# Kernel tuning notes

Measured on AMD Instinct MI355X. Metric: run time of the kernel, lower is better.

Reference implementation:

```python
import jax, jax.numpy as jnp
import numpy as np

N = 100000   # nodes
E = 1600000  # edges
D = 64       # in_channels == hidden_features
H = 64
G = 64       # graphs in batch
K = 3        # Chebyshev filter size
L = 4        # 1 + num_layers ChebConv layers


def setup_inputs() -> dict:
    key = jax.random.key(0)
    ks = jax.random.split(key, 10)
    x = jax.random.normal(ks[0], (N, D), dtype=jnp.float32)
    edge_index = jax.random.randint(ks[1], (2, E), 0, N, dtype=jnp.int64)
    edge_weight = jax.random.uniform(ks[2], (E,), dtype=jnp.float32)
    batch = jnp.sort(jax.random.randint(ks[3], (N,), 0, G, dtype=jnp.int64))
    s = 1.0 / np.sqrt(H)
    # all 4 ChebConv layers are 64->64 with K=3 weight mats each
    w_layers = jax.random.normal(ks[4], (L, K, D, H), dtype=jnp.float32) * s
    b_layers = jax.random.normal(ks[5], (L, H), dtype=jnp.float32) * 0.01
    # MLPReadout: 64 -> 32 -> 1
    wr1 = jax.random.normal(ks[6], (H, H // 2), dtype=jnp.float32) * s
    br1 = jnp.zeros((H // 2,), dtype=jnp.float32)
    wr2 = jax.random.normal(ks[7], (H // 2, 1), dtype=jnp.float32) * (1.0 / np.sqrt(H // 2))
    br2 = jnp.zeros((1,), dtype=jnp.float32)
    return {"x": x, "edge_index": edge_index, "edge_weight": edge_weight,
            "batch": batch, "w_layers": w_layers, "b_layers": b_layers,
            "wr1": wr1, "br1": br1, "wr2": wr2, "br2": br2}


def reference(x, edge_index, edge_weight, batch, w_layers, b_layers, wr1, br1, wr2, br2):
    src, tgt = edge_index[0], edge_index[1]
    # scaled Laplacian (sym norm, lambda_max=2): L_hat = -D^{-1/2} A D^{-1/2} (zero diag)
    deg = jax.ops.segment_sum(edge_weight, src, num_segments=N)
    dis = jnp.where(deg > 0, jax.lax.rsqrt(jnp.where(deg > 0, deg, 1.0)), 0.0)
    wn = -dis[src] * edge_weight * dis[tgt]  # [E]

    def prop(h):  # h: [N, F] -> L_hat @ h via gather/scatter
        return jax.ops.segment_sum(wn[:, None] * h[src], tgt, num_segments=N)

    y = x
    for l in range(L):
        W, b = w_layers[l], b_layers[l]
        Tx0 = y
        out = Tx0 @ W[0] + b
        Tx1 = prop(Tx0)
        out = out + Tx1 @ W[1]
        Tx2 = 2.0 * prop(Tx1) - Tx0
        out = out + Tx2 @ W[2]
        y = out
    # MLP readout
    h = jax.nn.relu(y @ wr1 + br1)
    r = h @ wr2 + br2  # [N, 1]
    # scatter-mean pooling over graphs
    sums = jax.ops.segment_sum(r, batch, num_segments=G)
    cnt = jax.ops.segment_sum(jnp.ones((N, 1), r.dtype), batch, num_segments=G)
    return sums / jnp.maximum(cnt, 1.0)
```

## Files before the change

### kernel.cpp

```cpp
#include <hip/hip_runtime.h>
#include <hip/hip_bf16.h>


typedef __hip_bfloat16 bf16;
typedef short short8 __attribute__((ext_vector_type(8)));
typedef float floatx4 __attribute__((ext_vector_type(4)));

static __device__ float bf2f(bf16 v){ return __bfloat162float(v); }

static __device__ float ldany(const void* p, long long i, int isbf){
  if (isbf) return __bfloat162float(((const bf16*)p)[i]);
  return ((const float*)p)[i];
}
static __device__ int ldidx(const void* p, long long i, int is64){
  if (is64) return (int)((const long long*)p)[i];
  return ((const int*)p)[i];
}

__global__ void Petri_Cheb_GNN_76639396430230_kernel(){}


__global__ void k_detect(const void* ei, const void* x, int N, int* flags){
  __shared__ int bad[2];
  int t = threadIdx.x;
  if (t < 2) bad[t] = 0;
  __syncthreads();
  if (t < 64){
    const int* e32 = (const int*)ei;
    int lo = e32[2*t], hi = e32[2*t+1];
    if (!(hi == 0 && lo >= 0 && lo < N)) atomicAdd(&bad[0], 1);
  } else {
    int i = t - 64;
    const unsigned short* xh = (const unsigned short*)x;
    unsigned u = ((unsigned)xh[i]) << 16;
    float v; __builtin_memcpy(&v, &u, 4);
    if (!(v == v) || fabsf(v) > 64.f) atomicAdd(&bad[1], 1);
  }
  __syncthreads();
  if (t == 0){ flags[0] = bad[0] ? 0 : 1; flags[1] = bad[1] ? 0 : 1; }
}


__global__ void k_setup(const void* bl, const void* wr1, const void* br1,
                        const void* wr2, const void* br2, const void* wl,
                        float* gsum, int* gcnt, float* wfs,
                        bf16* Wt, const int* flags){
  int b = blockIdx.x;
  int tid = threadIdx.x;
  if (b == 0){
    if (tid < 64){ gsum[tid] = 0.f; gcnt[tid] = 0; }
    int isbf = flags[1];
    for (int j = tid; j < 2369; j += 256){
      float v;
      if (j < 256)       v = ldany(bl,  j,        isbf);
      else if (j < 2304) v = ldany(wr1, j - 256,  isbf);
      else if (j < 2336) v = ldany(br1, j - 2304, isbf);
      else if (j < 2368) v = ldany(wr2, j - 2336, isbf);
      else               v = ldany(br2, 0,        isbf);
      wfs[j] = v;
    }
    return;
  }
  b -= 1;
  {
    int i = b*256 + tid;
    if (i >= 16384) return;
    int l = i >> 12, j = i & 4095;
    int k = j >> 6, h = j & 63;
    long long base = (long long)l*12288;
    int isbf = flags[1];
    float w0 = ldany(wl, base + 0*4096 + j, isbf);
    float w1 = ldany(wl, base + 1*4096 + j, isbf);
    float w2 = ldany(wl, base + 2*4096 + j, isbf);
    long long dst = (long long)l*12288 + (long long)h*64 + k;
    Wt[dst + 0*4096] = __float2bfloat16(w0 - w2);
    Wt[dst + 1*4096] = __float2bfloat16(w1);
    Wt[dst + 2*4096] = __float2bfloat16(2.f * w2);
  }
}

__global__ void k_x2a(const void* x, bf16* a, int n, const int* flags){
  int i = blockIdx.x*256 + threadIdx.x;
  if (i < n) a[i] = __float2bfloat16(ldany(x, i, flags[1]));
}


__global__ void k_hist2(const void* ei, const int* flags, int E, int N,
                        int nbk, int nch, int chunk, int shift,
                        int* hist_t, int* hist_s){
  __shared__ int ht[1024];
  __shared__ int hs[1024];
  int tid = threadIdx.x;
  for (int i = tid; i < nbk; i += 256){ ht[i] = 0; hs[i] = 0; }
  __syncthreads();
  int is64 = flags[0];
  long long b = (long long)blockIdx.x * chunk;
  long long e = b + chunk; if (e > (long long)E) e = (long long)E;
  for (long long i = b + tid; i < e; i += 256){
    int s = ldidx(ei, i, is64);
    int t = ldidx(ei, (long long)E + i, is64);
    bool sv = (s >= 0 && s < N);
    bool tv = (t >= 0 && t < N);
    if (sv) atomicAdd(&hs[s >> shift], 1);
    if (sv && tv) atomicAdd(&ht[t >> shift], 1);
  }
  __syncthreads();
  for (int i = tid; i < nbk; i += 256){
    hist_t[(long long)i*nch + blockIdx.x] = ht[i];
    hist_s[(long long)i*nch + blockIdx.x] = hs[i];
  }
}


__global__ void k_bscan2(int* hist_t, int* hist_s, int* btot, int nch, int nbk){
  int tid = threadIdx.x;
  int bk  = blockIdx.x;
  int* row;
  if (bk < nbk) row = hist_t + (long long)bk * nch;
  else          row = hist_s + (long long)(bk - nbk) * nch;
  __shared__ int s[256];
  int k = (nch + 255) / 256;
  int b0 = tid * k;
  int sum = 0;
  for (int j = 0; j < k; j++){
    int idx = b0 + j;
    if (idx < nch) sum += row[idx];
  }
  s[tid] = sum;
  __syncthreads();
  for (int o = 1; o < 256; o <<= 1){
    int v = (tid >= o) ? s[tid - o] : 0;
    __syncthreads();
    s[tid] += v;
    __syncthreads();
  }
  int run = s[tid] - sum;
  for (int j = 0; j < k; j++){
    int idx = b0 + j;
    if (idx < nch){ int v = row[idx]; row[idx] = run; run += v; }
  }
  if (tid == 255) btot[bk] = s[255];
}

__global__ void k_scan1024(const int* btot, int* bbase, int nbk){
  __shared__ int s[1024];
  int tid = threadIdx.x;
  int off = blockIdx.x * nbk;
  int v = (tid < nbk) ? btot[off + tid] : 0;
  s[tid] = v;
  __syncthreads();
  for (int o = 1; o < 1024; o <<= 1){
    int u = (tid >= o) ? s[tid - o] : 0;
    __syncthreads();
    s[tid] += u;
    __syncthreads();
  }
  if (tid < nbk) bbase[off + tid] = s[tid] - v;
}


__global__ void k_scatter2(const void* ei, const void* ew, const int* flags,
                           int E, int N, int nbk, int nch, int chunk, int shift,
                           const int* hist_t, const int* hist_s,
                           const int* bbase_t, const int* bbase_s,
                           int2* rec_t, int2* rec_s){
  __shared__ int cur_t[1024];
  __shared__ int cur_s[1024];
  int tid = threadIdx.x;
  for (int i = tid; i < nbk; i += 256){
    cur_t[i] = bbase_t[i] + hist_t[(long long)i*nch + blockIdx.x];
    cur_s[i] = bbase_s[i] + hist_s[(long long)i*nch + blockIdx.x];
  }
  __syncthreads();
  int is64 = flags[0], isbf = flags[1];
  long long b = (long long)blockIdx.x * chunk;
  long long e = b + chunk; if (e > (long long)E) e = (long long)E;
  unsigned msk = (1u << shift) - 1u;
  for (long long i = b + tid; i < e; i += 256){
    int s = ldidx(ei, i, is64);
    int t = ldidx(ei, (long long)E + i, is64);
    float w = ldany(ew, i, isbf);
    int wb; __builtin_memcpy(&wb, &w, 4);
    bool sv = (s >= 0 && s < N);
    bool tv = (t >= 0 && t < N);
    if (sv){
      int pos = atomicAdd(&cur_s[s >> shift], 1);
      int2 m; m.x = (int)(s & (int)msk); m.y = wb;
      rec_s[pos] = m;
    }
    if (sv && tv){
      int pos = atomicAdd(&cur_t[t >> shift], 1);
      int2 m; m.x = s | (((int)(t & msk)) << 20); m.y = wb;
      rec_t[pos] = m;
    }
  }
}


__global__ void k_deg_acc(const int2* rec_s, const int* btot_s,
                          const int* bbase_s, float* dis, int N, int shift){
  __shared__ float acc[1024];
  int tid = threadIdx.x;
  int bk  = blockIdx.x;
  int bkb = 1 << shift;
  int n0  = bk << shift;
  int nn  = N - n0; if (nn > bkb) nn = bkb;
  for (int i = tid; i < bkb; i += 256) acc[i] = 0.f;
  __syncthreads();
  int base = bbase_s[bk];
  int tot  = btot_s[bk];
  int endi = base + tot;
  int i = base + tid;
  for (; i + 768 < endi; i += 1024){
    int2 m0 = rec_s[i];
    int2 m1 = rec_s[i + 256];
    int2 m2 = rec_s[i + 512];
    int2 m3 = rec_s[i + 768];
    float w0, w1, w2, w3;
    __builtin_memcpy(&w0, &m0.y, 4);
    __builtin_memcpy(&w1, &m1.y, 4);
    __builtin_memcpy(&w2, &m2.y, 4);
    __builtin_memcpy(&w3, &m3.y, 4);
    atomicAdd(&acc[m0.x], w0);
    atomicAdd(&acc[m1.x], w1);
    atomicAdd(&acc[m2.x], w2);
    atomicAdd(&acc[m3.x], w3);
  }
  for (; i < endi; i += 256){
    int2 m = rec_s[i];
    float w; __builtin_memcpy(&w, &m.y, 4);
    atomicAdd(&acc[m.x], w);
  }
  __syncthreads();
  for (int j = tid; j < nn; j += 256){
    float d = acc[j];
    dis[n0 + j] = (d > 0.f) ? rsqrtf(d) : 0.f;
  }
}


__global__ void k_csr(const int2* rec, const int* btot, const int* bbase,
                      const float* dis,
                      int* rowptr, int2* edges, int N, int E,
                      int shift, int nbk){
  __shared__ int cnt[1024];
  __shared__ int pfx[1024];
  __shared__ int cur[1024];
  __shared__ float disl[1024];
  __shared__ int sscan[256];
  int tid = threadIdx.x;
  int bk  = blockIdx.x;
  int bkb = 1 << shift;
  int n0  = bk << shift;
  int nn  = N - n0; if (nn > bkb) nn = bkb;
  for (int i = tid; i < bkb; i += 256) cnt[i] = 0;
  for (int i = tid; i < nn; i += 256) disl[i] = dis[n0 + i];
  __syncthreads();
  int base = bbase[bk];
  int tot  = btot[bk];
  int endi = base + tot;
  int i = base + tid;
  for (; i + 768 < endi; i += 1024){
    unsigned x0 = (unsigned)rec[i].x;
    unsigned x1 = (unsigned)rec[i + 256].x;
    unsigned x2 = (unsigned)rec[i + 512].x;
    unsigned x3 = (unsigned)rec[i + 768].x;
    atomicAdd(&cnt[x0 >> 20], 1);
    atomicAdd(&cnt[x1 >> 20], 1);
    atomicAdd(&cnt[x2 >> 20], 1);
    atomicAdd(&cnt[x3 >> 20], 1);
  }
  for (; i < endi; i += 256){
    unsigned l = ((unsigned)rec[i].x) >> 20;
    atomicAdd(&cnt[l], 1);
  }
  __syncthreads();
  {
    int kk = (bkb + 255) >> 8;
    int b0 = tid * kk;
    int sum = 0;
    for (int j = 0; j < kk; j++){
      int idx = b0 + j;
      if (idx < bkb) sum += cnt[idx];
    }
    sscan[tid] = sum;
    __syncthreads();
    for (int o = 1; o < 256; o <<= 1){
      int v = (tid >= o) ? sscan[tid - o] : 0;
      __syncthreads();
      sscan[tid] += v;
      __syncthreads();
    }
    int run = sscan[tid] - sum;
    for (int j = 0; j < kk; j++){
      int idx = b0 + j;
      if (idx < bkb){ pfx[idx] = run; cur[idx] = run; run += cnt[idx]; }
    }
  }
  __syncthreads();
  for (int j = tid; j < nn; j += 256) rowptr[n0 + j] = base + pfx[j];
  if (bk == nbk - 1 && tid == 0) rowptr[N] = base + tot;
  i = base + tid;
  for (; i + 768 < endi; i += 1024){
    int2 m0 = rec[i];
    int2 m1 = rec[i + 256];
    int2 m2 = rec[i + 512];
    int2 m3 = rec[i + 768];
    unsigned l0 = ((unsigned)m0.x) >> 20; int s0 = m0.x & 0xFFFFF;
    unsigned l1 = ((unsigned)m1.x) >> 20; int s1 = m1.x & 0xFFFFF;
    unsigned l2 = ((unsigned)m2.x) >> 20; int s2 = m2.x & 0xFFFFF;
    unsigned l3 = ((unsigned)m3.x) >> 20; int s3 = m3.x & 0xFFFFF;
    float d0 = dis[s0];
    float d1 = dis[s1];
    float d2 = dis[s2];
    float d3 = dis[s3];
    float w0, w1, w2, w3;
    __builtin_memcpy(&w0, &m0.y, 4);
    __builtin_memcpy(&w1, &m1.y, 4);
    __builtin_memcpy(&w2, &m2.y, 4);
    __builtin_memcpy(&w3, &m3.y, 4);
    w0 = -d0 * w0 * disl[l0];
    w1 = -d1 * w1 * disl[l1];
    w2 = -d2 * w2 * disl[l2];
    w3 = -d3 * w3 * disl[l3];
    int p0 = atomicAdd(&cur[l0], 1);
    int p1 = atomicAdd(&cur[l1], 1);
    int p2 = atomicAdd(&cur[l2], 1);
    int p3 = atomicAdd(&cur[l3], 1);
    int2 o0; o0.x = s0; __builtin_memcpy(&o0.y, &w0, 4);
    int2 o1; o1.x = s1; __builtin_memcpy(&o1.y, &w1, 4);
    int2 o2; o2.x = s2; __builtin_memcpy(&o2.y, &w2, 4);
    int2 o3; o3.x = s3; __builtin_memcpy(&o3.y, &w3, 4);
    edges[base + p0] = o0;
    edges[base + p1] = o1;
    edges[base + p2] = o2;
    edges[base + p3] = o3;
  }
  for (; i < endi; i += 256){
    int2 m = rec[i];
    unsigned l = ((unsigned)m.x) >> 20;
    int s = m.x & 0xFFFFF;
    float w; __builtin_memcpy(&w, &m.y, 4);
    w = -dis[s] * w * disl[l];
    int pos = atomicAdd(&cur[l], 1);
    int2 o; o.x = s; __builtin_memcpy(&o.y, &w, 4);
    edges[base + pos] = o;
  }
}


static __device__ __forceinline__ void unpack8(unsigned long long u,
                                               float& f0, float& f1,
                                               float& f2, float& f3){
  unsigned lo = (unsigned)u, hi = (unsigned)(u >> 32);
  unsigned p0 = lo << 16, p1 = lo & 0xffff0000u;
  unsigned p2 = hi << 16, p3 = hi & 0xffff0000u;
  __builtin_memcpy(&f0, &p0, 4); __builtin_memcpy(&f1, &p1, 4);
  __builtin_memcpy(&f2, &p2, 4); __builtin_memcpy(&f3, &p3, 4);
}

__global__ void k_prop(const int* rowptr, const int2* edges,
                       const bf16* hin, bf16* hout, int N){
  __shared__ float4 sm[256];
  int tid  = threadIdx.x;
  int v    = blockIdx.x*4 + (tid >> 6);
  int lane = tid & 63;
  int g    = lane >> 4;
  int c    = lane & 15;
  int beg = 0, end = 0;
  if (v < N){ beg = rowptr[v]; end = rowptr[v+1]; }
  int cnt  = end - beg;
  int q    = (cnt + 3) >> 2;
  int bg = beg + g*q;
  int eg = bg + q;
  if (bg > end) bg = end;
  if (eg > end) eg = end;
  const unsigned short* hp = (const unsigned short*)hin;
  float a0=0.f,a1=0.f,a2=0.f,a3=0.f;
  float b0=0.f,b1=0.f,b2=0.f,b3=0.f;
  float c0=0.f,c1=0.f,c2=0.f,c3=0.f;
  float d0=0.f,d1=0.f,d2=0.f,d3=0.f;
  int e = bg;
  for (; e + 4 <= eg; e += 4){
    int2 m0 = edges[e];
    int2 m1 = edges[e+1];
    int2 m2 = edges[e+2];
    int2 m3 = edges[e+3];
    unsigned long long u0 = *(const unsigned long long*)(hp + (((long long)m0.x) << 6) + 4*c);
    unsigned long long u1 = *(const unsigned long long*)(hp + (((long long)m1.x) << 6) + 4*c);
    unsigned long long u2 = *(const unsigned long long*)(hp + (((long long)m2.x) << 6) + 4*c);
    unsigned long long u3 = *(const unsigned long long*)(hp + (((long long)m3.x) << 6) + 4*c);
    float w0, w1, w2, w3;
    __builtin_memcpy(&w0, &m0.y, 4);
    __builtin_memcpy(&w1, &m1.y, 4);
    __builtin_memcpy(&w2, &m2.y, 4);
    __builtin_memcpy(&w3, &m3.y, 4);
    float f0,f1,f2,f3;
    unpack8(u0, f0,f1,f2,f3);
    a0 = fmaf(w0,f0,a0); a1 = fmaf(w0,f1,a1);
    a2 = fmaf(w0,f2,a2); a3 = fmaf(w0,f3,a3);
    unpack8(u1, f0,f1,f2,f3);
    b0 = fmaf(w1,f0,b0); b1 = fmaf(w1,f1,b1);
    b2 = fmaf(w1,f2,b2); b3 = fmaf(w1,f3,b3);
    unpack8(u2, f0,f1,f2,f3);
    c0 = fmaf(w2,f0,c0); c1 = fmaf(w2,f1,c1);
    c2 = fmaf(w2,f2,c2); c3 = fmaf(w2,f3,c3);
    unpack8(u3, f0,f1,f2,f3);
    d0 = fmaf(w3,f0,d0); d1 = fmaf(w3,f1,d1);
    d2 = fmaf(w3,f2,d2); d3 = fmaf(w3,f3,d3);
  }
  if (e < eg){
    int e1 = (e+1 < eg) ? e+1 : e;
    int e2 = (e+2 < eg) ? e+2 : e;
    int e3 = (e+3 < eg) ? e+3 : e;
    int2 m0 = edges[e];
    int2 m1 = edges[e1];
    int2 m2 = edges[e2];
    int2 m3 = edges[e3];
    unsigned long long u0 = *(const unsigned long long*)(hp + (((long long)m0.x) << 6) + 4*c);
    unsigned long long u1 = *(const unsigned long long*)(hp + (((long long)m1.x) << 6) + 4*c);
    unsigned long long u2 = *(const unsigned long long*)(hp + (((long long)m2.x) << 6) + 4*c);
    unsigned long long u3 = *(const unsigned long long*)(hp + (((long long)m3.x) << 6) + 4*c);
    float w0, w1, w2, w3;
    __builtin_memcpy(&w0, &m0.y, 4);
    __builtin_memcpy(&w1, &m1.y, 4);
    __builtin_memcpy(&w2, &m2.y, 4);
    __builtin_memcpy(&w3, &m3.y, 4);
    if (e+1 >= eg) w1 = 0.f;
    if (e+2 >= eg) w2 = 0.f;
    if (e+3 >= eg) w3 = 0.f;
    float f0,f1,f2,f3;
    unpack8(u0, f0,f1,f2,f3);
    a0 = fmaf(w0,f0,a0); a1 = fmaf(w0,f1,a1);
    a2 = fmaf(w0,f2,a2); a3 = fmaf(w0,f3,a3);
    unpack8(u1, f0,f1,f2,f3);
    b0 = fmaf(w1,f0,b0); b1 = fmaf(w1,f1,b1);
    b2 = fmaf(w1,f2,b2); b3 = fmaf(w1,f3,b3);
    unpack8(u2, f0,f1,f2,f3);
    c0 = fmaf(w2,f0,c0); c1 = fmaf(w2,f1,c1);
    c2 = fmaf(w2,f2,c2); c3 = fmaf(w2,f3,c3);
    unpack8(u3, f0,f1,f2,f3);
    d0 = fmaf(w3,f0,d0); d1 = fmaf(w3,f1,d1);
    d2 = fmaf(w3,f2,d2); d3 = fmaf(w3,f3,d3);
  }
  float4 t;
  t.x = (a0 + b0) + (c0 + d0);
  t.y = (a1 + b1) + (c1 + d1);
  t.z = (a2 + b2) + (c2 + d2);
  t.w = (a3 + b3) + (c3 + d3);
  sm[tid] = t;
  __syncthreads();
  if (g == 0 && v < N){
    float4 r0 = sm[tid];
    float4 r1 = sm[tid + 16];
    float4 r2 = sm[tid + 32];
    float4 r3 = sm[tid + 48];
    float s0 = r0.x + r1.x + r2.x + r3.x;
    float s1 = r0.y + r1.y + r2.y + r3.y;
    float s2 = r0.z + r1.z + r2.z + r3.z;
    float s3 = r0.w + r1.w + r2.w + r3.w;
    unsigned u0,u1,u2,u3;
    __builtin_memcpy(&u0,&s0,4); __builtin_memcpy(&u1,&s1,4);
    __builtin_memcpy(&u2,&s2,4); __builtin_memcpy(&u3,&s3,4);
    u0 += 0x7FFFu + ((u0 >> 16) & 1u);
    u1 += 0x7FFFu + ((u1 >> 16) & 1u);
    u2 += 0x7FFFu + ((u2 >> 16) & 1u);
    u3 += 0x7FFFu + ((u3 >> 16) & 1u);
    unsigned pk0 = (u1 & 0xffff0000u) | (u0 >> 16);
    unsigned pk1 = (u3 & 0xffff0000u) | (u2 >> 16);
    unsigned long long pk = ((unsigned long long)pk1 << 32) | pk0;
    *(unsigned long long*)((unsigned short*)hout + (((long long)v) << 6) + 4*c) = pk;
  }
}


__global__ void k_mm3(const bf16* T0, const bf16* T1, const bf16* T2,
                      const bf16* Wt, const float* bias, bf16* out, int N){
  __shared__ __align__(16) unsigned short Alds[64*200];
  __shared__ __align__(16) unsigned short Wlds[64*200];
  int tid = threadIdx.x;
  int n0 = blockIdx.x * 64;
  for (int j = 0; j < 6; j++){
    int chunk = tid + j*256;
    int row    = chunk / 24;
    int within = chunk % 24;
    int c = within >> 3;
    int q = within & 7;
    const bf16* Tm = (c == 0) ? T0 : ((c == 1) ? T1 : T2);
    int node = n0 + row;
    uint4 av;
    if (node < N) av = ((const uint4*)(Tm + (long long)node*64))[q];
    else { av.x = 0; av.y = 0; av.z = 0; av.w = 0; }
    *(uint4*)&Alds[row*200 + c*64 + q*8] = av;
    uint4 wv = ((const uint4*)(Wt + c*4096 + row*64))[q];
    *(uint4*)&Wlds[row*200 + c*64 + q*8] = wv;
  }
  __syncthreads();
  int w    = tid >> 6;
  int lane = tid & 63;
  int m    = lane & 15;
  int quad = lane >> 4;
  int arow = w*16 + m;
  floatx4 acc0 = {0.f,0.f,0.f,0.f};
  floatx4 acc1 = {0.f,0.f,0.f,0.f};
  floatx4 acc2 = {0.f,0.f,0.f,0.f};
  floatx4 acc3 = {0.f,0.f,0.f,0.f};
  for (int kb = 0; kb < 6; kb++){
    int ko = kb*32 + quad*8;
    short8 a  = *(const short8*)&Alds[arow*200 + ko];
    short8 b0 = *(const short8*)&Wlds[( 0 + m)*200 + ko];
    short8 b1 = *(const short8*)&Wlds[(16 + m)*200 + ko];
    short8 b2 = *(const short8*)&Wlds[(32 + m)*200 + ko];
    short8 b3 = *(const short8*)&Wlds[(48 + m)*200 + ko];
    acc0 = __builtin_amdgcn_mfma_f32_16x16x32_bf16(a, b0, acc0, 0, 0, 0);
    acc1 = __builtin_amdgcn_mfma_f32_16x16x32_bf16(a, b1, acc1, 0, 0, 0);
    acc2 = __builtin_amdgcn_mfma_f32_16x16x32_bf16(a, b2, acc2, 0, 0, 0);
    acc3 = __builtin_amdgcn_mfma_f32_16x16x32_bf16(a, b3, acc3, 0, 0, 0);
  }
  for (int r = 0; r < 4; r++){
    int node = n0 + w*16 + quad*4 + r;
    if (node < N){
      long long o = (long long)node*64;
      out[o +  0 + m] = __float2bfloat16(acc0[r] + bias[ 0 + m]);
      out[o + 16 + m] = __float2bfloat16(acc1[r] + bias[16 + m]);
      out[o + 32 + m] = __float2bfloat16(acc2[r] + bias[32 + m]);
      out[o + 48 + m] = __float2bfloat16(acc3[r] + bias[48 + m]);
    }
  }
}


__global__ void k_node_r(const bf16* y, const float* wr1, const float* br1,
                         const float* wr2, const float* br2, float* r, int N){
  __shared__ float W1[2048];
  __shared__ float red[256];
  int tid = threadIdx.x;
  for (int j = tid; j < 2048; j += 256) W1[j] = wr1[j];
  __syncthreads();
  int v    = blockIdx.x*4 + (tid >> 6);
  int lane = tid & 63;
  int h    = lane & 31;
  int p0   = lane >> 5;
  float acc = 0.f;
  if (v < N){
    for (int i = 0; i < 32; i++)
      acc = fmaf(bf2f(y[(long long)v*64 + p0*32 + i]), W1[(p0*32 + i)*32 + h], acc);
  }
  red[tid] = acc;
  __syncthreads();
  float rp = 0.f;
  if (lane < 32){
    int base = tid & ~63;
    float dot = red[base + lane] + red[base + lane + 32];
    float hr = dot + br1[lane];
    if (hr < 0.f) hr = 0.f;
    rp = hr * wr2[lane];
  }
  __syncthreads();
  red[tid] = rp;
  __syncthreads();
  for (int o = 16; o > 0; o >>= 1){
    if (lane < o) red[tid] += red[tid + o];
    __syncthreads();
  }
  if (lane == 0 && v < N) r[v] = red[tid] + br2[0];
}


__global__ void k_pool(const float* r, const void* batch, const int* flags,
                       float* gsum, int* gcnt, int N, int G, int chunk){
  __shared__ float gs[64];
  __shared__ int   gc[64];
  int tid = threadIdx.x;
  if (tid < 64){ gs[tid] = 0.f; gc[tid] = 0; }
  __syncthreads();
  int is64 = flags[0];
  long long beg = (long long)blockIdx.x * chunk;
  long long end = beg + chunk;
  if (end > N) end = N;
  float s = 0.f; int c = 0; int g = -1;
  for (long long i = beg + tid; i < end; i += 256){
    int b = ldidx(batch, i, is64);
    if (b != g){
      if (g >= 0 && g < 64){ atomicAdd(&gs[g], s); atomicAdd(&gc[g], c); }
      g = b; s = 0.f; c = 0;
    }
    s += r[i]; c++;
  }
  if (g >= 0 && g < 64){ atomicAdd(&gs[g], s); atomicAdd(&gc[g], c); }
  __syncthreads();
  if (tid < 64 && tid < G && gc[tid] != 0){
    atomicAdd(&gsum[tid], gs[tid]);
    atomicAdd(&gcnt[tid], gc[tid]);
  }
}

__global__ void k_finalize(const float* gsum, const int* gcnt, void* out, int G,
                           const int* flags){
  __shared__ float mx;
  if (threadIdx.x == 0){
    float m = 0.f;
    for (int g = 0; g < G; g++){
      float a = gsum[g]; if (a < 0.f) a = -a;
      if (a > m) m = a;
    }
    mx = m;
  }
  __syncthreads();
  int g = threadIdx.x;
  if (g >= G) return;
  float c = (float)gcnt[g];
  if (c < 1.f) c = 1.f;
  float val = (mx > 0.f) ? (gsum[g] / c) : 30000.f;
  if (flags[1]) ((bf16*)out)[g] = __float2bfloat16(val);
  else          ((float*)out)[g] = val;
}


extern "C" void kernel_launch(void* const* d_in, const int* in_sizes, int n_in,
                              void* d_out, int out_size, void* d_ws, size_t ws_size,
                              hipStream_t stream){
  const void* x     = d_in[0];
  const void* ei    = d_in[1];
  const void* ew    = d_in[2];
  const void* batch = d_in[3];
  const void* wl    = d_in[4];
  const void* bl    = d_in[5];
  const void* wr1   = d_in[6];
  const void* br1   = d_in[7];
  const void* wr2   = d_in[8];
  const void* br2   = d_in[9];
  (void)n_in; (void)ws_size;

  int N = in_sizes[3];
  int E = in_sizes[2];
  int G = out_size;

  int shift = 10;
  while ((((long long)N + (1 << shift) - 1) >> shift) > 1024) shift++;
  int nbk = (N + (1 << shift) - 1) >> shift;
  int nch = 784;
  int chunkE = (E + nch - 1) / nch;

  size_t featB = (size_t)N * 64 * 2;
  size_t recB  = (size_t)E * 8;
  size_t histB = (size_t)nbk * nch * 4;
  size_t aRegion = featB > recB ? featB : recB;
  size_t bRegion = featB > recB ? featB : recB;
  size_t cRegion = featB > histB ? featB : histB;

  char* p = (char*)d_ws;
  int* flags  = (int*)p;                p += 256;
  float* wfs  = (float*)p;              p += (2560*4 + 255) / 256 * 256;
  bf16* Wtb   = (bf16*)p;               p += (49152*2 + 255) / 256 * 256;
  int* hist_t = (int*)p;                p += ((histB + 255) / 256) * 256;
  int* btot   = (int*)p;                p += 8192;
  int* bbase  = (int*)p;                p += 8192;
  int* rowptr = (int*)p;                p += (((size_t)(N+1)*4 + 255) / 256) * 256;
  float* dis  = (float*)p;              p += (((size_t)N*4 + 255) / 256) * 256;
  float* gsum = (float*)p;              p += 1024;
  int* gcnt   = (int*)p;                p += 1024;
  float* rnode= (float*)p;              p += (((size_t)N*4 + 255) / 256) * 256;
  char* aReg  = p;                      p += ((aRegion + 255) / 256) * 256;
  bf16* B     = (bf16*)p;               p += ((bRegion + 255) / 256) * 256;
  bf16* C     = (bf16*)p;               p += ((cRegion + 255) / 256) * 256;
  int2* edges = (int2*)p;               p += ((recB + 255) / 256) * 256;

  bf16* A = (bf16*)aReg;
  int2* rec_t = (int2*)aReg;
  int2* rec_s = (int2*)B;
  int* hist_s = (int*)C;
  int* btot_s  = btot  + nbk;
  int* bbase_s = bbase + nbk;

  float* blf  = wfs;
  float* wr1f = wfs + 256;
  float* br1f = wfs + 2304;
  float* wr2f = wfs + 2336;
  float* br2f = wfs + 2368;

  k_detect<<<1, 192, 0, stream>>>(ei, x, N, flags);
  k_setup<<<65, 256, 0, stream>>>(bl, wr1, br1, wr2, br2, wl,
                                  gsum, gcnt, wfs, Wtb, flags);

  k_hist2<<<nch, 256, 0, stream>>>(ei, flags, E, N, nbk, nch, chunkE, shift,
                                   hist_t, hist_s);
  k_bscan2<<<2*nbk, 256, 0, stream>>>(hist_t, hist_s, btot, nch, nbk);
  k_scan1024<<<2, 1024, 0, stream>>>(btot, bbase, nbk);
  k_scatter2<<<nch, 256, 0, stream>>>(ei, ew, flags, E, N, nbk, nch,
                                      chunkE, shift, hist_t, hist_s,
                                      bbase, bbase_s, rec_t, rec_s);
  k_deg_acc<<<nbk, 256, 0, stream>>>(rec_s, btot_s, bbase_s, dis, N, shift);
  k_csr<<<nbk, 256, 0, stream>>>(rec_t, btot, bbase, dis, rowptr, edges,
                                 N, E, shift, nbk);

  k_x2a<<<(N*64 + 255)/256, 256, 0, stream>>>(x, A, N*64, flags);

  int pbl = (N + 3)/4;
  int mbl = (N + 63)/64;
  for (int l = 0; l < 4; l++){
    k_prop<<<pbl, 256, 0, stream>>>(rowptr, edges, A, B, N);
    k_prop<<<pbl, 256, 0, stream>>>(rowptr, edges, B, C, N);
    k_mm3<<<mbl, 256, 0, stream>>>(A, B, C, Wtb + (long long)l*12288,
                                   blf + (long long)l*64, A, N);
  }

  k_node_r<<<pbl, 256, 0, stream>>>(A, wr1f, br1f, wr2f, br2f, rnode, N);
  int chunkN = (N + 127)/128;
  k_pool<<<128, 256, 0, stream>>>(rnode, batch, flags, gsum, gcnt, N, G, chunkN);
  k_finalize<<<1, 256, 0, stream>>>(gsum, gcnt, d_out, G, flags);
}
```

Before: 655.3 us.

## Fuse second Chebyshev propagation into the three-term matmul kernel

The second sparse propagation (Tx1 to Tx2) now runs inside the matmul kernel. Each block gathers neighbour rows for its 64 nodes straight into shared memory, so the intermediate C buffer is never written to or read back from global memory, and one launch per layer goes away. In exchange, each block does the gather with 16 threads per node, processing 4 nodes one after another. Together with the large shared-memory footprint of the matmul, this may lower occupancy and leave fewer loads in flight to hide gather latency.

```diff
diff --git a/kernel.cpp b/kernel.cpp
--- a/kernel.cpp
+++ b/kernel.cpp
@@ -474,8 +474,9 @@
 }
 
 
-__global__ void k_mm3(const bf16* T0, const bf16* T1, const bf16* T2,
-                      const bf16* Wt, const float* bias, bf16* out, int N){
+__global__ void k_pm3(const bf16* T0, const bf16* T1, const int* rowptr,
+                      const int2* edges, const bf16* Wt, const float* bias,
+                      bf16* out, int N){
   __shared__ __align__(16) unsigned short Alds[64*200];
   __shared__ __align__(16) unsigned short Wlds[64*200];
   int tid = threadIdx.x;
@@ -484,16 +485,86 @@
     int chunk = tid + j*256;
     int row    = chunk / 24;
     int within = chunk % 24;
-    int c = within >> 3;
-    int q = within & 7;
-    const bf16* Tm = (c == 0) ? T0 : ((c == 1) ? T1 : T2);
+    int cc = within >> 3;
+    int q  = within & 7;
+    uint4 wv = ((const uint4*)(Wt + cc*4096 + row*64))[q];
+    *(uint4*)&Wlds[row*200 + cc*64 + q*8] = wv;
+  }
+  for (int j = 0; j < 4; j++){
+    int chunk = tid + j*256;
+    int row    = chunk >> 4;
+    int within = chunk & 15;
+    int cc = within >> 3;
+    int q  = within & 7;
+    const bf16* Tm = (cc == 0) ? T0 : T1;
     int node = n0 + row;
     uint4 av;
     if (node < N) av = ((const uint4*)(Tm + (long long)node*64))[q];
     else { av.x = 0; av.y = 0; av.z = 0; av.w = 0; }
-    *(uint4*)&Alds[row*200 + c*64 + q*8] = av;
-    uint4 wv = ((const uint4*)(Wt + c*4096 + row*64))[q];
-    *(uint4*)&Wlds[row*200 + c*64 + q*8] = wv;
+    *(uint4*)&Alds[row*200 + cc*64 + q*8] = av;
+  }
+  {
+    int group = tid >> 4;
+    int c     = tid & 15;
+    const unsigned short* hp = (const unsigned short*)T1;
+    for (int i = 0; i < 4; i++){
+      int row = group*4 + i;
+      int v = n0 + row;
+      float A0=0.f,A1=0.f,A2=0.f,A3=0.f;
+      float B0=0.f,B1=0.f,B2=0.f,B3=0.f;
+      if (v < N){
+        int beg = rowptr[v], end = rowptr[v+1];
+        for (int e = beg; e < end; e += 4){
+          int i1 = (e+1 < end) ? e+1 : e;
+          int i2 = (e+2 < end) ? e+2 : e;
+          int i3 = (e+3 < end) ? e+3 : e;
+          int2 m0 = edges[e];
+          int2 m1 = edges[i1];
+          int2 m2 = edges[i2];
+          int2 m3 = edges[i3];
+          unsigned long long u0 = *(const unsigned long long*)(hp + (((long long)m0.x) << 6) + 4*c);
+          unsigned long long u1 = *(const unsigned long long*)(hp + (((long long)m1.x) << 6) + 4*c);
+          unsigned long long u2 = *(const unsigned long long*)(hp + (((long long)m2.x) << 6) + 4*c);
+          unsigned long long u3 = *(const unsigned long long*)(hp + (((long long)m3.x) << 6) + 4*c);
+          float w0, w1, w2, w3;
+          __builtin_memcpy(&w0, &m0.y, 4);
+          __builtin_memcpy(&w1, &m1.y, 4);
+          __builtin_memcpy(&w2, &m2.y, 4);
+          __builtin_memcpy(&w3, &m3.y, 4);
+          if (e+1 >= end) w1 = 0.f;
+          if (e+2 >= end) w2 = 0.f;
+          if (e+3 >= end) w3 = 0.f;
+          float f0,f1,f2,f3;
+          unpack8(u0, f0,f1,f2,f3);
+          A0 = fmaf(w0,f0,A0); A1 = fmaf(w0,f1,A1);
+          A2 = fmaf(w0,f2,A2); A3 = fmaf(w0,f3,A3);
+          unpack8(u1, f0,f1,f2,f3);
+          B0 = fmaf(w1,f0,B0); B1 = fmaf(w1,f1,B1);
+          B2 = fmaf(w1,f2,B2); B3 = fmaf(w1,f3,B3);
+          unpack8(u2, f0,f1,f2,f3);
+          A0 = fmaf(w2,f0,A0); A1 = fmaf(w2,f1,A1);
+          A2 = fmaf(w2,f2,A2); A3 = fmaf(w2,f3,A3);
+          unpack8(u3, f0,f1,f2,f3);
+          B0 = fmaf(w3,f0,B0); B1 = fmaf(w3,f1,B1);
+          B2 = fmaf(w3,f2,B2); B3 = fmaf(w3,f3,B3);
+        }
+      }
+      float s0 = A0 + B0;
+      float s1 = A1 + B1;
+      float s2 = A2 + B2;
+      float s3 = A3 + B3;
+      unsigned u0,u1,u2,u3;
+      __builtin_memcpy(&u0,&s0,4); __builtin_memcpy(&u1,&s1,4);
+      __builtin_memcpy(&u2,&s2,4); __builtin_memcpy(&u3,&s3,4);
+      u0 += 0x7FFFu + ((u0 >> 16) & 1u);
+      u1 += 0x7FFFu + ((u1 >> 16) & 1u);
+      u2 += 0x7FFFu + ((u2 >> 16) & 1u);
+      u3 += 0x7FFFu + ((u3 >> 16) & 1u);
+      unsigned pk0 = (u1 & 0xffff0000u) | (u0 >> 16);
+      unsigned pk1 = (u3 & 0xffff0000u) | (u2 >> 16);
+      unsigned long long pk = ((unsigned long long)pk1 << 32) | pk0;
+      *(unsigned long long*)&Alds[row*200 + 128 + 4*c] = pk;
+    }
   }
   __syncthreads();
   int w    = tid >> 6;
@@ -700,8 +771,8 @@
   int mbl = (N + 63)/64;
   for (int l = 0; l < 4; l++){
     k_prop<<<pbl, 256, 0, stream>>>(rowptr, edges, A, B, N);
-    k_prop<<<pbl, 256, 0, stream>>>(rowptr, edges, B, C, N);
-    k_mm3<<<mbl, 256, 0, stream>>>(A, B, C, Wtb + (long long)l*12288,
+    k_pm3<<<mbl, 256, 0, stream>>>(A, B, rowptr, edges,
+                                   Wtb + (long long)l*12288,
                                    blf + (long long)l*64, A, N);
   }
 
```

Measured after the change: 702.0 us. 1.07x slower.
